# Optimization experiments

Measured on AMD Instinct MI355X. Metric: run time of the kernel, lower is better.

## Reference

```python
import jax, jax.numpy as jnp
import numpy as np

HEADS = 8
C = 256            # in_channels == out_channels
NUM_STAR = 4
G = 32             # num graphs
N = 100000         # num nodes
LN_EPS = 1e-5


def setup_inputs() -> dict:
    key = jax.random.key(0)
    ks = jax.random.split(key, 9)
    stars = jax.random.normal(ks[0], (G, NUM_STAR, C), jnp.float32)
    nodes = jax.random.normal(ks[1], (N, C), jnp.float32)
    batch = jnp.sort(jax.random.randint(ks[2], (N,), 0, G))
    s = 1.0 / np.sqrt(C).astype(np.float32)
    Wq_w = jax.random.normal(ks[3], (C, C), jnp.float32) * s
    Wk_w = jax.random.normal(ks[4], (C, C), jnp.float32) * s
    Wv_w = jax.random.normal(ks[5], (C, C), jnp.float32) * s
    Wq_b = jnp.zeros((C,), jnp.float32)
    Wk_b = jnp.zeros((C,), jnp.float32)
    Wv_b = jnp.zeros((C,), jnp.float32)
    ln_gamma = jnp.ones((C,), jnp.float32)
    ln_beta = jnp.zeros((C,), jnp.float32)
    return dict(stars=stars, nodes=nodes, batch=batch,
                Wq_w=Wq_w, Wq_b=Wq_b, Wk_w=Wk_w, Wk_b=Wk_b,
                Wv_w=Wv_w, Wv_b=Wv_b, ln_gamma=ln_gamma, ln_beta=ln_beta)


def reference(stars, nodes, batch, Wq_w, Wq_b, Wk_w, Wk_b, Wv_w, Wv_b, ln_gamma, ln_beta):
    g, num_star, c = stars.shape
    n = nodes.shape[0]
    h = HEADS
    dh = c // h
    s_total = g * num_star                       # number of star nodes
    num_seg = n + s_total

    # x = [nodes; flattened stars]  (star index of (graph gidx, star i) = n + num_star*gidx + i)
    x = jnp.concatenate([nodes, stars.reshape(-1, c)], axis=0)     # [n+S, c]
    q = (x @ Wq_w.T + Wq_b).reshape(-1, h, dh)
    k = (x @ Wk_w.T + Wk_b).reshape(-1, h, dh)
    v = (x @ Wv_w.T + Wv_b).reshape(-1, h, dh)

    # edges: every node -> each of its graph's stars, plus star self-loops (use_star=True)
    rows = (n + num_star * batch[None, :] + jnp.arange(num_star)[:, None]).reshape(-1)  # [num_star*n]
    cols = jnp.broadcast_to(jnp.arange(n), (num_star, n)).reshape(-1)
    star_idx = jnp.arange(n, n + s_total)
    ei = jnp.concatenate([rows, star_idx])       # targets (query side)
    ej = jnp.concatenate([cols, star_idx])       # sources (key/value side)

    qe = q[ei]                                   # [E, h, dh]
    ke = k[ej]
    ve = v[ej]

    score = jnp.einsum('ehd,ehd->eh', qe, ke) / np.sqrt(dh).astype(np.float32)

    # segment softmax over target index (PyG-style, +1e-16 in denominator)
    m = jax.ops.segment_max(score, ei, num_segments=num_seg)
    m = jnp.where(jnp.isfinite(m), m, 0.0)       # empty segments -> 0
    ex = jnp.exp(score - m[ei])
    denom = jax.ops.segment_sum(ex, ei, num_segments=num_seg)
    coef = ex / (denom[ei] + 1e-16)              # [E, h]

    # dropout is identity in eval mode
    out = jax.ops.segment_sum(ve * coef[:, :, None], ei, num_segments=num_seg)  # [n+S, h, dh]
    new_stars = out[n:].reshape(g, num_star, c)

    new_stars = jax.nn.elu(new_stars)            # activation
    new_stars = new_stars + stars                # residual

    mu = jnp.mean(new_stars, axis=-1, keepdims=True)
    var = jnp.mean(jnp.square(new_stars - mu), axis=-1, keepdims=True)
    new_stars = (new_stars - mu) / jnp.sqrt(var + LN_EPS) * ln_gamma + ln_beta
    return new_stars
```

## Files before the change

kernel.cpp:

```cpp
#include <hip/hip_runtime.h>
#include <math.h>

#define HEADS 8
#define C 256
#define NUM_STAR 4
#define SLOTS 32
#define RSQRT_DH 0.17677669529663688f
#define LN_EPS 1e-5f
#define PF 8
#define CWK 16
#define RND 64
#define XB 264
#define UB 264
#define EP 40

typedef __attribute__((ext_vector_type(8))) short short8;
typedef __attribute__((ext_vector_type(4))) float floatx4;

__device__ __forceinline__ unsigned int f2b(float f) {
    unsigned int u = __float_as_uint(f);
    return (u + 0x7fffu + ((u >> 16) & 1u)) >> 16;
}

__global__ void k_gstart(const int* __restrict__ batch, int N, int G,
                         int* __restrict__ gstart) {
    int g = threadIdx.x;
    if (g > G) return;
    if (g == 0) { gstart[0] = 0; return; }
    if (g == G) { gstart[G] = N; return; }
    int lo = 0, hi = N;
    while (lo < hi) {
        int mid = (lo + hi) >> 1;
        if (batch[mid] < g) lo = mid + 1; else hi = mid;
    }
    gstart[g] = lo;
}

__global__ void k_star_prep(const float* __restrict__ stars,
                            const float* __restrict__ Wq_w, const float* __restrict__ Wq_b,
                            const float* __restrict__ Wk_w, const float* __restrict__ Wk_b,
                            unsigned short* __restrict__ U16, float* __restrict__ eself,
                            float* __restrict__ denom) {
    __shared__ float xs[C];
    __shared__ float qv[C];
    __shared__ float kv[C];
    const int gs = blockIdx.x;
    const int g = gs >> 2, s = gs & 3;
    const int t = threadIdx.x;

    xs[t] = stars[gs * C + t];
    __syncthreads();

    float aq = Wq_b[t], ak = Wk_b[t];
    const float* wq = Wq_w + (size_t)t * C;
    const float* wk = Wk_w + (size_t)t * C;
    #pragma unroll 4
    for (int j = 0; j < C; j += 4) {
        float4 x4 = *(const float4*)(xs + j);
        float4 a4 = *(const float4*)(wq + j);
        aq += a4.x * x4.x + a4.y * x4.y + a4.z * x4.z + a4.w * x4.w;
        float4 b4 = *(const float4*)(wk + j);
        ak += b4.x * x4.x + b4.y * x4.y + b4.z * x4.z + b4.w * x4.w;
    }
    qv[t] = aq; kv[t] = ak;
    __syncthreads();

    {
        float p = qv[t] * kv[t];
        #pragma unroll
        for (int off = 16; off; off >>= 1) p += __shfl_down(p, off, 32);
        if ((t & 31) == 0) {
            int h = t >> 5;
            float e = __expf(p * RSQRT_DH);
            eself[g * SLOTS + s * HEADS + h] = e;
            denom[g * SLOTS + s * HEADS + h] = e;
        }
    }

    {
        const int c = t;
        #pragma unroll
        for (int h = 0; h < HEADS; ++h) {
            float u = 0.f;
            for (int d = 0; d < 32; ++d)
                u += Wk_w[(size_t)(h * 32 + d) * C + c] * qv[h * 32 + d];
            U16[((size_t)g * SLOTS + s * HEADS + h) * C + c] =
                (unsigned short)f2b(u * RSQRT_DH);
        }
    }
}

__global__ __launch_bounds__(256, 2)
void k_fused(const float* __restrict__ nodes, const unsigned short* __restrict__ U16,
             const int* __restrict__ gstart, float* __restrict__ denom,
             float* __restrict__ Ypart) {
    __shared__ unsigned short u_lds[SLOTS * UB];
    __shared__ unsigned short x_lds[4 * CWK * XB];
    __shared__ unsigned short e_lds[2 * SLOTS * EP];

    const int g = blockIdx.x / PF, pb = blockIdx.x % PF;
    const int t = threadIdx.x;
    const int wv = t >> 6;
    const int l  = t & 63;
    const int lr = l & 15;
    const int q  = l >> 4;

    const int glo = gstart[g], ghi = gstart[g + 1];
    const int len = ghi - glo;
    const int L = (len + PF - 1) / PF;
    const int lo = glo + pb * L;
    const int hi = min(lo + L, ghi);
    const int nr = (hi > lo) ? (hi - lo + RND - 1) / RND : 0;

    {
        const unsigned short* ug = U16 + (size_t)g * SLOTS * C;
        #pragma unroll
        for (int i = 0; i < 8; ++i) {
            int r = wv * 8 + i;
            *(uint2*)&u_lds[r * UB + l * 4] = *(const uint2*)&ug[r * C + l * 4];
        }
    }

    const floatx4 z4 = {0.f, 0.f, 0.f, 0.f};
    floatx4 yacc[2][4];
    #pragma unroll
    for (int a = 0; a < 2; ++a)
        #pragma unroll
        for (int b = 0; b < 4; ++b) yacc[a][b] = z4;
    float dsum[8];
    #pragma unroll
    for (int i = 0; i < 8; ++i) dsum[i] = 0.f;

    unsigned short* xw = &x_lds[wv * CWK * XB];

    float4 xr[CWK];
    if (nr > 0) {
        int base = lo + wv * CWK;
        #pragma unroll
        for (int i = 0; i < CWK; ++i) {
            int gn = base + i;
            xr[i] = (gn < hi) ? *(const float4*)&nodes[(size_t)gn * C + l * 4]
                              : make_float4(0.f, 0.f, 0.f, 0.f);
        }
    }

    for (int rd = 0; rd < nr; ++rd) {
        __syncthreads();

        #pragma unroll
        for (int i = 0; i < CWK; ++i) {
            uint2 w;
            w.x = f2b(xr[i].x) | (f2b(xr[i].y) << 16);
            w.y = f2b(xr[i].z) | (f2b(xr[i].w) << 16);
            *(uint2*)&xw[i * XB + l * 4] = w;
        }
        if (rd + 1 < nr) {
            int base = lo + (rd + 1) * RND + wv * CWK;
            #pragma unroll
            for (int i = 0; i < CWK; ++i) {
                int gn = base + i;
                xr[i] = (gn < hi) ? *(const float4*)&nodes[(size_t)gn * C + l * 4]
                                  : make_float4(0.f, 0.f, 0.f, 0.f);
            }
        }

        floatx4 sacc0 = z4, sacc1 = z4;
        {
            const unsigned short* ur0 = &u_lds[lr * UB + q * 8];
            const unsigned short* ur1 = &u_lds[(16 + lr) * UB + q * 8];
            const unsigned short* xrw = &xw[lr * XB + q * 8];
            #pragma unroll
            for (int kt = 0; kt < 8; ++kt) {
                short8 a0 = *(const short8*)(ur0 + kt * 32);
                short8 a1 = *(const short8*)(ur1 + kt * 32);
                short8 bx = *(const short8*)(xrw + kt * 32);
                sacc0 = __builtin_amdgcn_mfma_f32_16x16x32_bf16(a0, bx, sacc0, 0, 0, 0);
                sacc1 = __builtin_amdgcn_mfma_f32_16x16x32_bf16(a1, bx, sacc1, 0, 0, 0);
            }
        }

        {
            int base = lo + rd * RND + wv * CWK;
            const bool valid = (base + lr) < hi;
            unsigned short* ew = &e_lds[(wv >> 1) * SLOTS * EP + (wv & 1) * 16 + lr];
            #pragma unroll
            for (int r = 0; r < 4; ++r) {
                float e0 = valid ? __expf(sacc0[r]) : 0.f;
                float e1 = valid ? __expf(sacc1[r]) : 0.f;
                dsum[r]     += e0;
                dsum[4 + r] += e1;
                ew[(q * 4 + r) * EP]        = (unsigned short)f2b(e0);
                ew[(16 + q * 4 + r) * EP]   = (unsigned short)f2b(e1);
            }
        }
        __syncthreads();

        #pragma unroll
        for (int p = 0; p < 2; ++p) {
            short8 pa0 = *(const short8*)&e_lds[(p * SLOTS + lr) * EP + q * 8];
            short8 pa1 = *(const short8*)&e_lds[(p * SLOTS + 16 + lr) * EP + q * 8];
            const unsigned short* xb0 =
                &x_lds[((p * 2 + (q >> 1)) * CWK + (q & 1) * 8) * XB + wv * 64 + lr];
            #pragma unroll
            for (int ct = 0; ct < 4; ++ct) {
                short8 bx;
                #pragma unroll
                for (int j = 0; j < 8; ++j) bx[j] = (short)xb0[j * XB + ct * 16];
                yacc[0][ct] = __builtin_amdgcn_mfma_f32_16x16x32_bf16(pa0, bx, yacc[0][ct], 0, 0, 0);
                yacc[1][ct] = __builtin_amdgcn_mfma_f32_16x16x32_bf16(pa1, bx, yacc[1][ct], 0, 0, 0);
            }
        }
    }

    {
        float* yg = &Ypart[(((size_t)g * PF + pb) * SLOTS) * C];
        #pragma unroll
        for (int st = 0; st < 2; ++st)
            #pragma unroll
            for (int ct = 0; ct < 4; ++ct)
                #pragma unroll
                for (int r = 0; r < 4; ++r)
                    yg[(st * 16 + q * 4 + r) * C + wv * 64 + ct * 16 + lr] = yacc[st][ct][r];
    }

    #pragma unroll
    for (int i = 0; i < 8; ++i) {
        float v = dsum[i];
        v += __shfl_xor(v, 1);
        v += __shfl_xor(v, 2);
        v += __shfl_xor(v, 4);
        v += __shfl_xor(v, 8);
        dsum[i] = v;
    }
    if (lr == 0) {
        #pragma unroll
        for (int mt = 0; mt < 2; ++mt)
            #pragma unroll
            for (int r = 0; r < 4; ++r)
                atomicAdd(&denom[g * SLOTS + mt * 16 + q * 4 + r], dsum[mt * 4 + r]);
    }
}

__global__ void k_epilogue(const float* __restrict__ stars,
                           const float* __restrict__ Wv_w, const float* __restrict__ Wv_b,
                           const float* __restrict__ gamma, const float* __restrict__ beta,
                           const float* __restrict__ Ypart, const float* __restrict__ eself,
                           const float* __restrict__ denom, float* __restrict__ out) {
    __shared__ float xs[C];
    __shared__ float yl[HEADS * C];
    __shared__ float cs[HEADS], ivd[HEADS], scl[HEADS];
    __shared__ float rb[8];

    const int gs = blockIdx.x;
    const int g = gs >> 2, s = gs & 3;
    const int t = threadIdx.x;

    xs[t] = stars[gs * C + t];
    if (t < HEADS) {
        float dn = denom[g * SLOTS + s * HEADS + t];
        float iv = 1.f / (dn + 1e-16f);
        ivd[t] = iv;
        cs[t] = eself[g * SLOTS + s * HEADS + t] * iv;
        scl[t] = dn * iv;
    }
    __syncthreads();

    for (int i = t; i < HEADS * C; i += 256) {
        int h = i >> 8, j = i & 255;
        float sum = 0.f;
        #pragma unroll
        for (int pbi = 0; pbi < PF; ++pbi)
            sum += Ypart[(((size_t)g * PF + pbi) * SLOTS + s * HEADS + h) * C + j];
        yl[i] = sum * ivd[h] + cs[h] * xs[j];
    }
    __syncthreads();

    const int c = t, h = c >> 5;
    float a = 0.f;
    const float* wv = Wv_w + (size_t)c * C;
    const float* yh = &yl[h * C];
    #pragma unroll 4
    for (int j = 0; j < C; j += 4) {
        float4 w4 = *(const float4*)(wv + j);
        float4 y4 = *(const float4*)(yh + j);
        a += w4.x * y4.x + w4.y * y4.y + w4.z * y4.z + w4.w * y4.w;
    }
    a += Wv_b[c] * scl[h];

    float v = a > 0.f ? a : (__expf(a) - 1.f);
    float r = v + xs[c];

    float ssum = r;
    #pragma unroll
    for (int off = 32; off; off >>= 1) ssum += __shfl_down(ssum, off, 64);
    const int wid = t >> 6, lane = t & 63;
    if (lane == 0) rb[wid] = ssum;
    __syncthreads();
    const float mu = (rb[0] + rb[1] + rb[2] + rb[3]) * (1.f / 256.f);
    const float d = r - mu;
    float vsum = d * d;
    #pragma unroll
    for (int off = 32; off; off >>= 1) vsum += __shfl_down(vsum, off, 64);
    if (lane == 0) rb[4 + wid] = vsum;
    __syncthreads();
    const float var = (rb[4] + rb[5] + rb[6] + rb[7]) * (1.f / 256.f);
    out[gs * C + c] = d * rsqrtf(var + LN_EPS) * gamma[c] + beta[c];
}

extern "C" void kernel_launch(void* const* d_in, const int* in_sizes, int n_in,
                              void* d_out, int out_size, void* d_ws, size_t ws_size,
                              hipStream_t stream) {
    const float* stars = (const float*)d_in[0];
    const float* nodes = (const float*)d_in[1];
    const int*   batch = (const int*)d_in[2];
    const float* Wq_w  = (const float*)d_in[3];
    const float* Wq_b  = (const float*)d_in[4];
    const float* Wk_w  = (const float*)d_in[5];
    const float* Wk_b  = (const float*)d_in[6];
    const float* Wv_w  = (const float*)d_in[7];
    const float* Wv_b  = (const float*)d_in[8];
    const float* gamma = (const float*)d_in[9];
    const float* beta  = (const float*)d_in[10];

    const int N = in_sizes[1] / C;
    const int G = in_sizes[0] / (NUM_STAR * C);

    unsigned short* U16 = (unsigned short*)d_ws;
    float* eself = (float*)((char*)d_ws + (size_t)G * SLOTS * C * 2);
    float* denom = eself + (size_t)G * SLOTS;
    float* Ypart = denom + (size_t)G * SLOTS;
    int*   gstart = (int*)(Ypart + (size_t)G * PF * SLOTS * C);

    float* out = (float*)d_out;

    k_gstart<<<1, 64, 0, stream>>>(batch, N, G, gstart);
    k_star_prep<<<G * NUM_STAR, 256, 0, stream>>>(stars, Wq_w, Wq_b, Wk_w, Wk_b,
                                                  U16, eself, denom);
    k_fused<<<G * PF, 256, 0, stream>>>(nodes, U16, gstart, denom, Ypart);
    k_epilogue<<<G * NUM_STAR, 256, 0, stream>>>(stars, Wv_w, Wv_b, gamma, beta,
                                                 Ypart, eself, denom, out);
}
```

Measured before the change: 73.67 us.

## Add transposed swizzled LDS copy of nodes, keep U in registers, merge gstart kernel

Writes a second, channel-major swizzled bf16 copy of each node tile into LDS. The second MFMA (e·X) can then load its B operand with one vector load instead of eight strided scalar LDS reads. The U matrix is held in registers rather than LDS, and PF is doubled to 16 to launch more blocks. The gstart binary search is folded into the star-prep kernel as an extra block, saving one launch. The costs are more register pressure, a larger LDS footprint and more Ypart partials for the epilogue to reduce.

```diff
diff --git a/kernel.cpp b/kernel.cpp
--- a/kernel.cpp
+++ b/kernel.cpp
@@ -7,11 +7,12 @@
 #define SLOTS 32
 #define RSQRT_DH 0.17677669529663688f
 #define LN_EPS 1e-5f
-#define PF 8
+#define PF 16
 #define CWK 16
 #define RND 64
 #define XB 264
-#define UB 264
+#define ST 40
+#define CNP (C * ST)
 #define EP 40
 
 typedef __attribute__((ext_vector_type(8))) short short8;
@@ -21,26 +22,31 @@
     unsigned int u = __float_as_uint(f);
     return (u + 0x7fffu + ((u >> 16) & 1u)) >> 16;
 }
-
-__global__ void k_gstart(const int* __restrict__ batch, int N, int G,
-                         int* __restrict__ gstart) {
-    int g = threadIdx.x;
-    if (g > G) return;
-    if (g == 0) { gstart[0] = 0; return; }
-    if (g == G) { gstart[G] = N; return; }
-    int lo = 0, hi = N;
-    while (lo < hi) {
-        int mid = (lo + hi) >> 1;
-        if (batch[mid] < g) lo = mid + 1; else hi = mid;
-    }
-    gstart[g] = lo;
+__device__ __forceinline__ float fcomp(const float4& v, int jj) {
+    return jj == 0 ? v.x : jj == 1 ? v.y : jj == 2 ? v.z : v.w;
 }
 
 __global__ void k_star_prep(const float* __restrict__ stars,
                             const float* __restrict__ Wq_w, const float* __restrict__ Wq_b,
                             const float* __restrict__ Wk_w, const float* __restrict__ Wk_b,
                             unsigned short* __restrict__ U16, float* __restrict__ eself,
-                            float* __restrict__ denom) {
+                            float* __restrict__ denom,
+                            const int* __restrict__ batch, int N, int G,
+                            int* __restrict__ gstart) {
+    if (blockIdx.x == gridDim.x - 1) {
+        int g = threadIdx.x;
+        if (g > G) return;
+        if (g == 0) { gstart[0] = 0; return; }
+        if (g == G) { gstart[G] = N; return; }
+        int lo = 0, hi = N;
+        while (lo < hi) {
+            int mid = (lo + hi) >> 1;
+            if (batch[mid] < g) lo = mid + 1; else hi = mid;
+        }
+        gstart[g] = lo;
+        return;
+    }
+
     __shared__ float xs[C];
     __shared__ float qv[C];
     __shared__ float kv[C];
@@ -94,8 +100,8 @@
 void k_fused(const float* __restrict__ nodes, const unsigned short* __restrict__ U16,
              const int* __restrict__ gstart, float* __restrict__ denom,
              float* __restrict__ Ypart) {
-    __shared__ unsigned short u_lds[SLOTS * UB];
-    __shared__ unsigned short x_lds[4 * CWK * XB];
+    __shared__ unsigned short x_nc[4 * CWK * XB];
+    __shared__ unsigned short x_cn[2 * CNP];
     __shared__ unsigned short e_lds[2 * SLOTS * EP];
 
     const int g = blockIdx.x / PF, pb = blockIdx.x % PF;
@@ -112,13 +118,14 @@
     const int hi = min(lo + L, ghi);
     const int nr = (hi > lo) ? (hi - lo + RND - 1) / RND : 0;
 
+    short8 ureg[2][8];
     {
         const unsigned short* ug = U16 + (size_t)g * SLOTS * C;
         #pragma unroll
-        for (int i = 0; i < 8; ++i) {
-            int r = wv * 8 + i;
-            *(uint2*)&u_lds[r * UB + l * 4] = *(const uint2*)&ug[r * C + l * 4];
-        }
+        for (int st2 = 0; st2 < 2; ++st2)
+            #pragma unroll
+            for (int kt = 0; kt < 8; ++kt)
+                ureg[st2][kt] = *(const short8*)&ug[(st2 * 16 + lr) * C + q * 8 + kt * 32];
     }
 
     const floatx4 z4 = {0.f, 0.f, 0.f, 0.f};
@@ -131,7 +138,8 @@
     #pragma unroll
     for (int i = 0; i < 8; ++i) dsum[i] = 0.f;
 
-    unsigned short* xw = &x_lds[wv * CWK * XB];
+    unsigned short* xw = &x_nc[wv * CWK * XB];
+    const int p_own = wv >> 1, hw = wv & 1;
 
     float4 xr[CWK];
     if (nr > 0) {
@@ -149,10 +157,27 @@
 
         #pragma unroll
         for (int i = 0; i < CWK; ++i) {
-            uint2 w;
-            w.x = f2b(xr[i].x) | (f2b(xr[i].y) << 16);
-            w.y = f2b(xr[i].z) | (f2b(xr[i].w) << 16);
-            *(uint2*)&xw[i * XB + l * 4] = w;
+            uint2 w2;
+            w2.x = f2b(xr[i].x) | (f2b(xr[i].y) << 16);
+            w2.y = f2b(xr[i].z) | (f2b(xr[i].w) << 16);
+            *(uint2*)&xw[i * XB + l * 4] = w2;
+        }
+        #pragma unroll
+        for (int jj = 0; jj < 4; ++jj) {
+            const int c = 4 * l + jj;
+            const int sz = ((c >> 2) ^ (c >> 4)) & 3;
+            uint4 ulo, uhi;
+            ulo.x = f2b(fcomp(xr[0], jj)) | (f2b(fcomp(xr[1], jj)) << 16);
+            ulo.y = f2b(fcomp(xr[2], jj)) | (f2b(fcomp(xr[3], jj)) << 16);
+            ulo.z = f2b(fcomp(xr[4], jj)) | (f2b(fcomp(xr[5], jj)) << 16);
+            ulo.w = f2b(fcomp(xr[6], jj)) | (f2b(fcomp(xr[7], jj)) << 16);
+            uhi.x = f2b(fcomp(xr[8], jj)) | (f2b(fcomp(xr[9], jj)) << 16);
+            uhi.y = f2b(fcomp(xr[10], jj)) | (f2b(fcomp(xr[11], jj)) << 16);
+            uhi.z = f2b(fcomp(xr[12], jj)) | (f2b(fcomp(xr[13], jj)) << 16);
+            uhi.w = f2b(fcomp(xr[14], jj)) | (f2b(fcomp(xr[15], jj)) << 16);
+            unsigned short* basep = &x_cn[p_own * CNP + c * ST];
+            *(uint4*)&basep[((hw * 2 + 0) ^ sz) * 8] = ulo;
+            *(uint4*)&basep[((hw * 2 + 1) ^ sz) * 8] = uhi;
         }
         if (rd + 1 < nr) {
             int base = lo + (rd + 1) * RND + wv * CWK;
@@ -166,31 +191,27 @@
 
         floatx4 sacc0 = z4, sacc1 = z4;
         {
-            const unsigned short* ur0 = &u_lds[lr * UB + q * 8];
-            const unsigned short* ur1 = &u_lds[(16 + lr) * UB + q * 8];
             const unsigned short* xrw = &xw[lr * XB + q * 8];
             #pragma unroll
             for (int kt = 0; kt < 8; ++kt) {
-                short8 a0 = *(const short8*)(ur0 + kt * 32);
-                short8 a1 = *(const short8*)(ur1 + kt * 32);
                 short8 bx = *(const short8*)(xrw + kt * 32);
-                sacc0 = __builtin_amdgcn_mfma_f32_16x16x32_bf16(a0, bx, sacc0, 0, 0, 0);
-                sacc1 = __builtin_amdgcn_mfma_f32_16x16x32_bf16(a1, bx, sacc1, 0, 0, 0);
+                sacc0 = __builtin_amdgcn_mfma_f32_16x16x32_bf16(ureg[0][kt], bx, sacc0, 0, 0, 0);
+                sacc1 = __builtin_amdgcn_mfma_f32_16x16x32_bf16(ureg[1][kt], bx, sacc1, 0, 0, 0);
             }
         }
 
         {
             int base = lo + rd * RND + wv * CWK;
             const bool valid = (base + lr) < hi;
-            unsigned short* ew = &e_lds[(wv >> 1) * SLOTS * EP + (wv & 1) * 16 + lr];
+            unsigned short* ew = &e_lds[p_own * SLOTS * EP + hw * 16 + lr];
             #pragma unroll
             for (int r = 0; r < 4; ++r) {
                 float e0 = valid ? __expf(sacc0[r]) : 0.f;
                 float e1 = valid ? __expf(sacc1[r]) : 0.f;
                 dsum[r]     += e0;
                 dsum[4 + r] += e1;
-                ew[(q * 4 + r) * EP]        = (unsigned short)f2b(e0);
-                ew[(16 + q * 4 + r) * EP]   = (unsigned short)f2b(e1);
+                ew[(q * 4 + r) * EP]      = (unsigned short)f2b(e0);
+                ew[(16 + q * 4 + r) * EP] = (unsigned short)f2b(e1);
             }
         }
         __syncthreads();
@@ -199,13 +220,11 @@
         for (int p = 0; p < 2; ++p) {
             short8 pa0 = *(const short8*)&e_lds[(p * SLOTS + lr) * EP + q * 8];
             short8 pa1 = *(const short8*)&e_lds[(p * SLOTS + 16 + lr) * EP + q * 8];
-            const unsigned short* xb0 =
-                &x_lds[((p * 2 + (q >> 1)) * CWK + (q & 1) * 8) * XB + wv * 64 + lr];
             #pragma unroll
             for (int ct = 0; ct < 4; ++ct) {
-                short8 bx;
-                #pragma unroll
-                for (int j = 0; j < 8; ++j) bx[j] = (short)xb0[j * XB + ct * 16];
+                const int c = wv * 64 + ct * 16 + lr;
+                const int sz = ((c >> 2) ^ (c >> 4)) & 3;
+                short8 bx = *(const short8*)&x_cn[p * CNP + c * ST + ((q ^ sz) * 8)];
                 yacc[0][ct] = __builtin_amdgcn_mfma_f32_16x16x32_bf16(pa0, bx, yacc[0][ct], 0, 0, 0);
                 yacc[1][ct] = __builtin_amdgcn_mfma_f32_16x16x32_bf16(pa1, bx, yacc[1][ct], 0, 0, 0);
             }
@@ -232,7 +251,7 @@
         v += __shfl_xor(v, 8);
         dsum[i] = v;
     }
-    if (lr == 0) {
+    if (lr == 0 && nr > 0) {
         #pragma unroll
         for (int mt = 0; mt < 2; ++mt)
             #pragma unroll
@@ -333,9 +352,9 @@
 
     float* out = (float*)d_out;
 
-    k_gstart<<<1, 64, 0, stream>>>(batch, N, G, gstart);
-    k_star_prep<<<G * NUM_STAR, 256, 0, stream>>>(stars, Wq_w, Wq_b, Wk_w, Wk_b,
-                                                  U16, eself, denom);
+    k_star_prep<<<G * NUM_STAR + 1, 256, 0, stream>>>(stars, Wq_w, Wq_b, Wk_w, Wk_b,
+                                                      U16, eself, denom,
+                                                      batch, N, G, gstart);
     k_fused<<<G * PF, 256, 0, stream>>>(nodes, U16, gstart, denom, Ypart);
     k_epilogue<<<G * NUM_STAR, 256, 0, stream>>>(stars, Wv_w, Wv_b, gamma, beta,
                                                  Ypart, eself, denom, out);
```

Result: no change. 73.04 us (-0.9%).
